# Performance work log

Hardware: AMD Instinct MI355X
Metric: run time of the kernel (lower is better)

## Reference

```python
import jax, jax.numpy as jnp
import numpy as np

N = 50000      # nodes per graph (= num hyperedges, forced by the stack ops)
E = 800000     # incidence pairs per graph
L = 16         # max nodes per hyperedge (padded with index 0)
F_IN = 128     # in_channels
D1 = 256       # dim_1
D2 = D1 // 4   # conv2 out dim = FusionAttention in_size
H_ATT = 128    # FusionAttention hidden_size
EPS = 1e-15


def setup_inputs() -> dict:
    key = jax.random.key(0)
    ks = jax.random.split(key, 32)
    inp = {}
    for i in range(4):
        inp[f"x{i}"] = jax.random.normal(ks[i], (N, F_IN), jnp.float32)
        nidx = jax.random.randint(ks[4 + i], (E,), 0, N, dtype=jnp.int32)
        eidx = jax.random.randint(ks[8 + i], (E,), 0, N, dtype=jnp.int32)
        inp[f"ei{i}"] = jnp.stack([nidx, eidx])  # [2, E]
        hn = jax.random.randint(ks[12 + i], (N, L), 0, N + 1, dtype=jnp.int32)
        inp[f"hnode{i}"] = hn
        # hye_len = number of real (non-padding) entries per hyperedge
        inp[f"hlen{i}"] = jnp.sum(hn > 0, axis=1, keepdims=True).astype(jnp.float32)
    # shared Hgnn params (PyG HypergraphConv: lin without bias + separate bias)
    inp["W1"] = jax.random.normal(ks[16], (F_IN, D1), jnp.float32) / np.sqrt(F_IN).astype(np.float32)
    inp["b1"] = jnp.zeros((D1,), jnp.float32)
    inp["W2"] = jax.random.normal(ks[17], (D1, D2), jnp.float32) / np.sqrt(D1).astype(np.float32)
    inp["b2"] = jnp.zeros((D2,), jnp.float32)
    # two FusionAttention heads: Linear(D2,H_ATT)+Tanh, Linear(H_ATT,1,bias=False)
    for name, a, b in [("ac", 18, 19), ("am", 20, 21)]:
        inp[f"{name}_W1"] = jax.random.normal(ks[a], (D2, H_ATT), jnp.float32) / np.sqrt(D2).astype(np.float32)
        inp[f"{name}_b1"] = jnp.zeros((H_ATT,), jnp.float32)
        inp[f"{name}_W2"] = jax.random.normal(ks[b], (H_ATT, 1), jnp.float32) / np.sqrt(H_ATT).astype(np.float32)
    return inp


def _hconv(x, node_idx, edge_idx, W, b):
    """PyG HypergraphConv (heads=1, unit hyperedge weights):
    X' = D^-1 H B^-1 H^T (X W) + b, via two segment-sum passes."""
    x = x @ W  # [N, out]
    ones = jnp.ones(node_idx.shape, x.dtype)
    deg_n = jax.ops.segment_sum(ones, node_idx, num_segments=N)
    d_inv = jnp.where(deg_n > 0, 1.0 / deg_n, 0.0)
    deg_e = jax.ops.segment_sum(ones, edge_idx, num_segments=N)
    b_inv = jnp.where(deg_e > 0, 1.0 / deg_e, 0.0)
    # node -> hyperedge: m_e = B^-1[e] * sum_{v in e} x[v]
    efeat = b_inv[:, None] * jax.ops.segment_sum(x[node_idx], edge_idx, num_segments=N)
    # hyperedge -> node: out_v = D^-1[v] * sum_{e : v in e} m_e
    out = d_inv[:, None] * jax.ops.segment_sum(efeat[edge_idx], node_idx, num_segments=N)
    return out + b


def _hgnn(x, ei, W1, b1, W2, b2):
    x = jax.nn.relu(_hconv(x, ei[0], ei[1], W1, b1))
    return jax.nn.relu(_hconv(x, ei[0], ei[1], W2, b2))


def _hye_emb(node_emb, hlen, hnode):
    # prepend zero row so padding index 0 gathers zeros
    padded = jnp.concatenate([jnp.zeros((1, node_emb.shape[1]), node_emb.dtype), node_emb], axis=0)
    seq = padded[hnode]                    # [M, L, F]
    return jnp.sum(seq, axis=1) / (hlen + EPS)


def _fusion_attn(z, W1, b1, W2):
    # z: [N, 4, d]
    w = (jnp.tanh(z @ W1 + b1) @ W2).mean(0)      # [4, 1]
    beta = jax.nn.softmax(w, axis=0)              # [4, 1]
    return jnp.sum(beta * z, axis=1)              # [N, d]


def reference(x0, x1, x2, x3, ei0, ei1, ei2, ei3,
              hlen0, hlen1, hlen2, hlen3, hnode0, hnode1, hnode2, hnode3,
              W1, b1, W2, b2, ac_W1, ac_b1, ac_W2, am_W1, am_b1, am_W2):
    x1_cm = _hgnn(x0, ei0, W1, b1, W2, b2)
    x1_mc = _hgnn(x1, ei1, W1, b1, W2, b2)
    x1_cc = _hgnn(x2, ei2, W1, b1, W2, b2)
    x1_mm = _hgnn(x3, ei3, W1, b1, W2, b2)
    x2_cm = _hye_emb(x1_cm, hlen0, hnode0)
    x2_mc = _hye_emb(x1_mc, hlen1, hnode1)
    x2_cc = _hye_emb(x1_cc, hlen2, hnode2)
    x2_mm = _hye_emb(x1_mm, hlen3, hnode3)
    x_c = jnp.stack((x1_mc, x2_cm, x1_cc, x2_cc), axis=1)  # [N, 4, D2]
    x_m = jnp.stack((x1_cm, x2_mc, x1_mm, x2_mm), axis=1)
    h_c = _fusion_attn(x_c, ac_W1, ac_b1, ac_W2)
    h_m = _fusion_attn(x_m, am_W1, am_b1, am_W2)
    return (h_c, h_m)
```

## Files before the change

### kernel.cpp

```cpp
#include <hip/hip_runtime.h>
#include <hip/hip_bf16.h>

#define NF   128
#define DD1  256
#define DD2  64
#define HATT 128

static inline int cdiv(int a, int b) { return (a + b - 1) / b; }

__global__ __launch_bounds__(256) void count_rank(const int* __restrict__ nidx,
                                                  const int* __restrict__ eidx,
                                                  int* __restrict__ deg,
                                                  int* __restrict__ rank,
                                                  int N, int E) {
    int e = blockIdx.x * 256 + threadIdx.x;
    if (e < E) {
        const int vn = nidx[e], ve = eidx[e];
        const int rn = atomicAdd(&deg[vn], 1);
        const int re = atomicAdd(&deg[N + ve], 1);
        rank[e] = rn | (re << 16);
    }
}

__global__ __launch_bounds__(256) void scan_blocks(const int* __restrict__ in,
                                                   int* __restrict__ out,
                                                   int* __restrict__ partials, int n) {
    __shared__ int s[256];
    const int base = blockIdx.x * 1024;
    const int t = threadIdx.x;
    int v[4], sum = 0;
#pragma unroll
    for (int i = 0; i < 4; i++) {
        const int idx = base + t * 4 + i;
        v[i] = (idx < n) ? in[idx] : 0;
        sum += v[i];
    }
    s[t] = sum;
    __syncthreads();
    for (int o = 1; o < 256; o <<= 1) {
        int x = 0;
        if (t >= o) x = s[t - o];
        __syncthreads();
        if (t >= o) s[t] += x;
        __syncthreads();
    }
    if (t == 255) partials[blockIdx.x] = s[255];
    int run = (t == 0) ? 0 : s[t - 1];
#pragma unroll
    for (int i = 0; i < 4; i++) {
        const int idx = base + t * 4 + i;
        if (idx < n) out[idx] = run;
        run += v[i];
    }
}

__global__ __launch_bounds__(256) void scan_partials(int* __restrict__ partials, int P) {
    __shared__ int s[256];
    const int t = threadIdx.x;
    s[t] = (t < P) ? partials[t] : 0;
    __syncthreads();
    for (int o = 1; o < 256; o <<= 1) {
        int x = 0;
        if (t >= o) x = s[t - o];
        __syncthreads();
        if (t >= o) s[t] += x;
        __syncthreads();
    }
    if (t < P) partials[t] = (t == 0) ? 0 : s[t - 1];
}

__global__ __launch_bounds__(256) void scan_add(int* __restrict__ off,
                                                const int* __restrict__ partials,
                                                int n, int total) {
    const int idx = blockIdx.x * 256 + threadIdx.x;
    if (idx < n) off[idx] += partials[idx >> 10];
    if (idx == 0) off[n] = total;
}

__global__ __launch_bounds__(256) void build_fill(const int* __restrict__ nidx,
                                                  const int* __restrict__ eidx,
                                                  const int* __restrict__ rank,
                                                  const int* __restrict__ off,
                                                  int* __restrict__ srcidx,
                                                  int N, int E, int shardSize) {
    const int shard = blockIdx.x & 7;
    const int chunk = blockIdx.x >> 3;
    const int lo = shard * shardSize;
    const int hi = lo + shardSize;
    const int base = chunk * 1024;
#pragma unroll
    for (int i = 0; i < 4; i++) {
        const int e = base + i * 256 + threadIdx.x;
        if (e < E) {
            const int vn = nidx[e], ve = eidx[e];
            const int rk = rank[e];
            if (vn >= lo && vn < hi)
                srcidx[off[vn] + (rk & 0xffff)] = ve;
            if (ve >= lo && ve < hi)
                srcidx[off[N + ve] + (rk >> 16)] = vn;
        }
    }
}

__global__ __launch_bounds__(256) void invert_deg_int(const int* __restrict__ deg,
                                                      float* __restrict__ inv, int n) {
    int t = blockIdx.x * 256 + threadIdx.x;
    if (t < n) {
        const int v = deg[t];
        inv[t] = (v > 0) ? 1.0f / (float)v : 0.f;
    }
}

__global__ __launch_bounds__(256) void gather_rows_128(const float* __restrict__ src,
                                                       const int* __restrict__ off,
                                                       const int* __restrict__ srcidx,
                                                       const float* __restrict__ scale,
                                                       float* __restrict__ dst, int Nn) {
    const int row = blockIdx.x * 16 + (threadIdx.x >> 4);
    if (row >= Nn) return;
    const int c = (threadIdx.x & 15) << 2;
    const int j0 = off[row], j1 = off[row + 1];
    float4 pa = make_float4(0.f, 0.f, 0.f, 0.f);
    float4 pb = make_float4(0.f, 0.f, 0.f, 0.f);
    float4 qa = make_float4(0.f, 0.f, 0.f, 0.f);
    float4 qb = make_float4(0.f, 0.f, 0.f, 0.f);
    int j = j0;
    for (; j + 3 < j1; j += 4) {
        const int s0 = srcidx[j + 0];
        const int s1 = srcidx[j + 1];
        const int s2 = srcidx[j + 2];
        const int s3 = srcidx[j + 3];
        const float4 v0a = *(const float4*)&src[(size_t)s0 * 128 + c];
        const float4 v0b = *(const float4*)&src[(size_t)s0 * 128 + c + 64];
        const float4 v1a = *(const float4*)&src[(size_t)s1 * 128 + c];
        const float4 v1b = *(const float4*)&src[(size_t)s1 * 128 + c + 64];
        const float4 v2a = *(const float4*)&src[(size_t)s2 * 128 + c];
        const float4 v2b = *(const float4*)&src[(size_t)s2 * 128 + c + 64];
        const float4 v3a = *(const float4*)&src[(size_t)s3 * 128 + c];
        const float4 v3b = *(const float4*)&src[(size_t)s3 * 128 + c + 64];
        pa.x += v0a.x + v1a.x; pa.y += v0a.y + v1a.y;
        pa.z += v0a.z + v1a.z; pa.w += v0a.w + v1a.w;
        qa.x += v2a.x + v3a.x; qa.y += v2a.y + v3a.y;
        qa.z += v2a.z + v3a.z; qa.w += v2a.w + v3a.w;
        pb.x += v0b.x + v1b.x; pb.y += v0b.y + v1b.y;
        pb.z += v0b.z + v1b.z; pb.w += v0b.w + v1b.w;
        qb.x += v2b.x + v3b.x; qb.y += v2b.y + v3b.y;
        qb.z += v2b.z + v3b.z; qb.w += v2b.w + v3b.w;
    }
    for (; j < j1; j++) {
        const int s0 = srcidx[j];
        const float4 va = *(const float4*)&src[(size_t)s0 * 128 + c];
        const float4 vb = *(const float4*)&src[(size_t)s0 * 128 + c + 64];
        pa.x += va.x; pa.y += va.y; pa.z += va.z; pa.w += va.w;
        pb.x += vb.x; pb.y += vb.y; pb.z += vb.z; pb.w += vb.w;
    }
    float4 aca = make_float4(pa.x + qa.x, pa.y + qa.y, pa.z + qa.z, pa.w + qa.w);
    float4 acb = make_float4(pb.x + qb.x, pb.y + qb.y, pb.z + qb.z, pb.w + qb.w);
    if (scale) {
        const float s = scale[row];
        aca.x *= s; aca.y *= s; aca.z *= s; aca.w *= s;
        acb.x *= s; acb.y *= s; acb.z *= s; acb.w *= s;
    }
    *(float4*)&dst[(size_t)row * 128 + c] = aca;
    *(float4*)&dst[(size_t)row * 128 + c + 64] = acb;
}

__global__ __launch_bounds__(256) void gather_rows_64(const float* __restrict__ src,
                                                      const int* __restrict__ off,
                                                      const int* __restrict__ srcidx,
                                                      const float* __restrict__ scale,
                                                      const float* __restrict__ post_bias,
                                                      float* __restrict__ dst, int Nn) {
    const int row = blockIdx.x * 32 + (threadIdx.x >> 3);
    if (row >= Nn) return;
    const int c = (threadIdx.x & 7) << 2;
    const int j0 = off[row], j1 = off[row + 1];
    float4 pa = make_float4(0.f, 0.f, 0.f, 0.f);
    float4 pb = make_float4(0.f, 0.f, 0.f, 0.f);
    float4 qa = make_float4(0.f, 0.f, 0.f, 0.f);
    float4 qb = make_float4(0.f, 0.f, 0.f, 0.f);
    int j = j0;
    for (; j + 3 < j1; j += 4) {
        const int s0 = srcidx[j + 0];
        const int s1 = srcidx[j + 1];
        const int s2 = srcidx[j + 2];
        const int s3 = srcidx[j + 3];
        const float4 v0a = *(const float4*)&src[(size_t)s0 * 64 + c];
        const float4 v0b = *(const float4*)&src[(size_t)s0 * 64 + c + 32];
        const float4 v1a = *(const float4*)&src[(size_t)s1 * 64 + c];
        const float4 v1b = *(const float4*)&src[(size_t)s1 * 64 + c + 32];
        const float4 v2a = *(const float4*)&src[(size_t)s2 * 64 + c];
        const float4 v2b = *(const float4*)&src[(size_t)s2 * 64 + c + 32];
        const float4 v3a = *(const float4*)&src[(size_t)s3 * 64 + c];
        const float4 v3b = *(const float4*)&src[(size_t)s3 * 64 + c + 32];
        pa.x += v0a.x + v1a.x; pa.y += v0a.y + v1a.y;
        pa.z += v0a.z + v1a.z; pa.w += v0a.w + v1a.w;
        qa.x += v2a.x + v3a.x; qa.y += v2a.y + v3a.y;
        qa.z += v2a.z + v3a.z; qa.w += v2a.w + v3a.w;
        pb.x += v0b.x + v1b.x; pb.y += v0b.y + v1b.y;
        pb.z += v0b.z + v1b.z; pb.w += v0b.w + v1b.w;
        qb.x += v2b.x + v3b.x; qb.y += v2b.y + v3b.y;
        qb.z += v2b.z + v3b.z; qb.w += v2b.w + v3b.w;
    }
    for (; j < j1; j++) {
        const int s0 = srcidx[j];
        const float4 va = *(const float4*)&src[(size_t)s0 * 64 + c];
        const float4 vb = *(const float4*)&src[(size_t)s0 * 64 + c + 32];
        pa.x += va.x; pa.y += va.y; pa.z += va.z; pa.w += va.w;
        pb.x += vb.x; pb.y += vb.y; pb.z += vb.z; pb.w += vb.w;
    }
    float4 aca = make_float4(pa.x + qa.x, pa.y + qa.y, pa.z + qa.z, pa.w + qa.w);
    float4 acb = make_float4(pb.x + qb.x, pb.y + qb.y, pb.z + qb.z, pb.w + qb.w);
    if (scale) {
        const float s = scale[row];
        aca.x *= s; aca.y *= s; aca.z *= s; aca.w *= s;
        acb.x *= s; acb.y *= s; acb.z *= s; acb.w *= s;
    }
    if (post_bias) {
        aca.x = fmaxf(aca.x + post_bias[c + 0], 0.f);
        aca.y = fmaxf(aca.y + post_bias[c + 1], 0.f);
        aca.z = fmaxf(aca.z + post_bias[c + 2], 0.f);
        aca.w = fmaxf(aca.w + post_bias[c + 3], 0.f);
        acb.x = fmaxf(acb.x + post_bias[c + 32], 0.f);
        acb.y = fmaxf(acb.y + post_bias[c + 33], 0.f);
        acb.z = fmaxf(acb.z + post_bias[c + 34], 0.f);
        acb.w = fmaxf(acb.w + post_bias[c + 35], 0.f);
    }
    *(float4*)&dst[(size_t)row * 64 + c] = aca;
    *(float4*)&dst[(size_t)row * 64 + c + 32] = acb;
}

__global__ __launch_bounds__(256) void gemm1_f32(const float* __restrict__ A,
                                                 const float* __restrict__ B,
                                                 float* __restrict__ C, int M,
                                                 const float* __restrict__ dinv,
                                                 const float* __restrict__ bias) {
    __shared__ float As[32][132];
    __shared__ float Bs[32][128];
    const int tid = threadIdx.x;
    const int m0 = blockIdx.y * 128;
    const int bn = blockIdx.x * 128;
    const int rq = (tid >> 4) << 2;
    const int cq = (tid & 15) << 2;

    float acc[8][8] = {{0.f}};

    for (int k0 = 0; k0 < 128; k0 += 32) {
#pragma unroll
        for (int i = 0; i < 4; i++) {
            const int f = tid + 256 * i;
            const int r = f >> 3;
            const int q = (f & 7) << 2;
            const int grow = m0 + r;
            float4 v = make_float4(0.f, 0.f, 0.f, 0.f);
            if (grow < M) v = *(const float4*)&A[(size_t)grow * 128 + k0 + q];
            As[q + 0][r] = v.x;
            As[q + 1][r] = v.y;
            As[q + 2][r] = v.z;
            As[q + 3][r] = v.w;
        }
#pragma unroll
        for (int i = 0; i < 4; i++) {
            const int f = tid + 256 * i;
            const int r = f >> 5;
            const int c4 = (f & 31) << 2;
            *(float4*)&Bs[r][c4] = *(const float4*)&B[(size_t)(k0 + r) * 256 + bn + c4];
        }
        __syncthreads();
#pragma unroll
        for (int k = 0; k < 32; k++) {
            float av[8], bv[8];
            *(float4*)&av[0] = *(const float4*)&As[k][rq];
            *(float4*)&av[4] = *(const float4*)&As[k][rq + 64];
            *(float4*)&bv[0] = *(const float4*)&Bs[k][cq];
            *(float4*)&bv[4] = *(const float4*)&Bs[k][cq + 64];
#pragma unroll
            for (int r = 0; r < 8; r++)
#pragma unroll
                for (int c = 0; c < 8; c++)
                    acc[r][c] = fmaf(av[r], bv[c], acc[r][c]);
        }
        __syncthreads();
    }
#pragma unroll
    for (int r = 0; r < 8; r++) {
        const int grow = m0 + rq + (r & 3) + ((r >> 2) << 6);
        if (grow < M) {
            const float s = dinv[grow];
            float o[8];
#pragma unroll
            for (int c = 0; c < 4; c++)
                o[c] = fmaxf(fmaf(acc[r][c], s, bias[bn + cq + c]), 0.f);
#pragma unroll
            for (int c = 4; c < 8; c++)
                o[c] = fmaxf(fmaf(acc[r][c], s, bias[bn + 64 + cq + (c - 4)]), 0.f);
            *(float4*)&C[(size_t)grow * 256 + bn + cq] = *(float4*)&o[0];
            *(float4*)&C[(size_t)grow * 256 + bn + 64 + cq] = *(float4*)&o[4];
        }
    }
}

__global__ __launch_bounds__(256) void gemm2_f32(const float* __restrict__ A,
                                                 const float* __restrict__ B,
                                                 float* __restrict__ C, int M) {
    __shared__ float As[32][132];
    __shared__ float Bs[32][64];
    const int tid = threadIdx.x;
    const int m0 = blockIdx.y * 128;
    const int tr = (tid >> 3) << 2;
    const int tc = (tid & 7) << 3;

    float acc[4][8] = {{0.f}};

    for (int k0 = 0; k0 < 256; k0 += 32) {
#pragma unroll
        for (int i = 0; i < 4; i++) {
            const int f = tid + 256 * i;
            const int r = f >> 3;
            const int q = (f & 7) << 2;
            const int grow = m0 + r;
            float4 v = make_float4(0.f, 0.f, 0.f, 0.f);
            if (grow < M) v = *(const float4*)&A[(size_t)grow * 256 + k0 + q];
            As[q + 0][r] = v.x;
            As[q + 1][r] = v.y;
            As[q + 2][r] = v.z;
            As[q + 3][r] = v.w;
        }
#pragma unroll
        for (int i = 0; i < 2; i++) {
            const int f = tid + 256 * i;
            const int r = f >> 4;
            const int c4 = (f & 15) << 2;
            *(float4*)&Bs[r][c4] = *(const float4*)&B[(size_t)(k0 + r) * 64 + c4];
        }
        __syncthreads();
#pragma unroll
        for (int k = 0; k < 32; k++) {
            float av[4], bv[8];
            *(float4*)&av[0] = *(const float4*)&As[k][tr];
            *(float4*)&bv[0] = *(const float4*)&Bs[k][tc];
            *(float4*)&bv[4] = *(const float4*)&Bs[k][tc + 4];
#pragma unroll
            for (int r = 0; r < 4; r++)
#pragma unroll
                for (int c = 0; c < 8; c++)
                    acc[r][c] = fmaf(av[r], bv[c], acc[r][c]);
        }
        __syncthreads();
    }
#pragma unroll
    for (int r = 0; r < 4; r++) {
        const int grow = m0 + tr + r;
        if (grow < M) {
            *(float4*)&C[(size_t)grow * 64 + tc] =
                make_float4(acc[r][0], acc[r][1], acc[r][2], acc[r][3]);
            *(float4*)&C[(size_t)grow * 64 + tc + 4] =
                make_float4(acc[r][4], acc[r][5], acc[r][6], acc[r][7]);
        }
    }
}

__global__ __launch_bounds__(256) void hye_emb_kernel(const float* __restrict__ emb,
                                                      const int* __restrict__ hnode,
                                                      const float* __restrict__ hlen,
                                                      float* __restrict__ out, int Nn) {
    const int r = blockIdx.x * 16 + (threadIdx.x >> 4);
    const int c = (threadIdx.x & 15) << 2;
    if (r >= Nn) return;
    const int4* hp4 = (const int4*)&hnode[(size_t)r * 16];
    const int4 w0 = hp4[0], w1 = hp4[1], w2 = hp4[2], w3 = hp4[3];
    int idx[16] = {w0.x, w0.y, w0.z, w0.w, w1.x, w1.y, w1.z, w1.w,
                   w2.x, w2.y, w2.z, w2.w, w3.x, w3.y, w3.z, w3.w};
    float4 a0 = make_float4(0.f, 0.f, 0.f, 0.f);
    float4 a1 = make_float4(0.f, 0.f, 0.f, 0.f);
    float4 a2 = make_float4(0.f, 0.f, 0.f, 0.f);
    float4 a3 = make_float4(0.f, 0.f, 0.f, 0.f);
#pragma unroll
    for (int l = 0; l < 16; l += 4) {
        if (idx[l + 0] > 0) {
            const float4 v = *(const float4*)&emb[(size_t)(idx[l + 0] - 1) * 64 + c];
            a0.x += v.x; a0.y += v.y; a0.z += v.z; a0.w += v.w;
        }
        if (idx[l + 1] > 0) {
            const float4 v = *(const float4*)&emb[(size_t)(idx[l + 1] - 1) * 64 + c];
            a1.x += v.x; a1.y += v.y; a1.z += v.z; a1.w += v.w;
        }
        if (idx[l + 2] > 0) {
            const float4 v = *(const float4*)&emb[(size_t)(idx[l + 2] - 1) * 64 + c];
            a2.x += v.x; a2.y += v.y; a2.z += v.z; a2.w += v.w;
        }
        if (idx[l + 3] > 0) {
            const float4 v = *(const float4*)&emb[(size_t)(idx[l + 3] - 1) * 64 + c];
            a3.x += v.x; a3.y += v.y; a3.z += v.z; a3.w += v.w;
        }
    }
    const float inv = 1.0f / (hlen[r] + 1e-15f);
    float4 acc;
    acc.x = (a0.x + a1.x + a2.x + a3.x) * inv;
    acc.y = (a0.y + a1.y + a2.y + a3.y) * inv;
    acc.z = (a0.z + a1.z + a2.z + a3.z) * inv;
    acc.w = (a0.w + a1.w + a2.w + a3.w) * inv;
    *(float4*)&out[(size_t)r * 64 + c] = acc;
}

struct AttnArgs {
    const float* z[8];
    const float* W1c; const float* b1c; const float* W2c;
    const float* W1m; const float* b1m; const float* W2m;
    float* accw;
    int Nn;
};

__global__ __launch_bounds__(256) void attn_gemm(AttnArgs a) {
    __shared__ float As[64][68];
    __shared__ float Bs[64][128];
    __shared__ float red[4];
    const int tid = threadIdx.x;
    const int gy = blockIdx.y;
    const int head = gy >> 2;
    const float* __restrict__ z  = a.z[gy];
    const float* __restrict__ W1 = head ? a.W1m : a.W1c;
    const float* __restrict__ b1 = head ? a.b1m : a.b1c;
    const float* __restrict__ W2 = head ? a.W2m : a.W2c;
    const int m0 = blockIdx.x * 64;

    {
        const int m = tid >> 2;
        const int qb = tid & 3;
        const int grow = m0 + m;
#pragma unroll
        for (int it = 0; it < 4; it++) {
            const int q = qb + 4 * it;
            float4 v = make_float4(0.f, 0.f, 0.f, 0.f);
            if (grow < a.Nn) v = *(const float4*)&z[(size_t)grow * 64 + q * 4];
            As[q * 4 + 0][m] = v.x;
            As[q * 4 + 1][m] = v.y;
            As[q * 4 + 2][m] = v.z;
            As[q * 4 + 3][m] = v.w;
        }
    }
    {
#pragma unroll
        for (int i = 0; i < 8; i++) {
            const int f = tid + 256 * i;
            const int r = f >> 5, cc = (f & 31) << 2;
            *(float4*)&Bs[r][cc] = *(const float4*)&W1[(size_t)r * 128 + cc];
        }
    }
    __syncthreads();

    const int mq = (tid & 15) << 2;
    const int cq = (tid >> 4) << 2;
    float acc[4][8] = {{0.f}};
    for (int k = 0; k < 64; k++) {
        float av[4], bv[8];
        *(float4*)&av[0] = *(const float4*)&As[k][mq];
        *(float4*)&bv[0] = *(const float4*)&Bs[k][cq];
        *(float4*)&bv[4] = *(const float4*)&Bs[k][cq + 64];
#pragma unroll
        for (int r = 0; r < 4; r++)
#pragma unroll
            for (int c = 0; c < 8; c++)
                acc[r][c] = fmaf(av[r], bv[c], acc[r][c]);
    }

    float w2v[8], b1v[8];
#pragma unroll
    for (int c = 0; c < 8; c++) {
        const int col = cq + (c & 3) + ((c >> 2) << 6);
        w2v[c] = W2[col];
        b1v[c] = b1[col];
    }
    float local = 0.f;
#pragma unroll
    for (int r = 0; r < 4; r++) {
        if (m0 + mq + r < a.Nn) {
#pragma unroll
            for (int c = 0; c < 8; c++) {
                float s = acc[r][c] + b1v[c];
                s = fminf(fmaxf(s, -15.f), 15.f);
                const float t = __expf(2.f * s);
                local += (1.f - 2.f / (t + 1.f)) * w2v[c];
            }
        }
    }
#pragma unroll
    for (int off = 32; off >= 1; off >>= 1) local += __shfl_down(local, off, 64);
    if ((tid & 63) == 0) red[tid >> 6] = local;
    __syncthreads();
    if (tid == 0) atomicAdd(&a.accw[gy], red[0] + red[1] + red[2] + red[3]);
}

__global__ void softmax_beta(const float* __restrict__ acc, float* __restrict__ beta,
                             float invN) {
    const int t = threadIdx.x;
    if (t < 2) {
        const float* a = acc + 4 * t;
        float* b = beta + 4 * t;
        float w[4], m = -1e30f;
#pragma unroll
        for (int i = 0; i < 4; i++) { w[i] = a[i] * invN; m = fmaxf(m, w[i]); }
        float s = 0.f;
#pragma unroll
        for (int i = 0; i < 4; i++) { w[i] = expf(w[i] - m); s += w[i]; }
#pragma unroll
        for (int i = 0; i < 4; i++) b[i] = w[i] / s;
    }
}

__global__ __launch_bounds__(256) void weighted_sum(const float* __restrict__ z0,
                                                    const float* __restrict__ z1,
                                                    const float* __restrict__ z2,
                                                    const float* __restrict__ z3,
                                                    const float* __restrict__ beta,
                                                    float* __restrict__ out, int Nn) {
    const int t = blockIdx.x * 256 + threadIdx.x;
    if (t >= Nn * 16) return;
    const float b0 = beta[0], b1 = beta[1], b2 = beta[2], b3 = beta[3];
    const float4 v0 = *(const float4*)&z0[(size_t)t * 4];
    const float4 v1 = *(const float4*)&z1[(size_t)t * 4];
    const float4 v2 = *(const float4*)&z2[(size_t)t * 4];
    const float4 v3 = *(const float4*)&z3[(size_t)t * 4];
    float4 o;
    o.x = b0 * v0.x + b1 * v1.x + b2 * v2.x + b3 * v3.x;
    o.y = b0 * v0.y + b1 * v1.y + b2 * v2.y + b3 * v3.y;
    o.z = b0 * v0.z + b1 * v1.z + b2 * v2.z + b3 * v3.z;
    o.w = b0 * v0.w + b1 * v1.w + b2 * v2.w + b3 * v3.w;
    *(float4*)&out[(size_t)t * 4] = o;
}

extern "C" void kernel_launch(void* const* d_in, const int* in_sizes, int n_in,
                              void* d_out, int out_size, void* d_ws, size_t ws_size,
                              hipStream_t stream) {
    const int Nn = in_sizes[0] / NF;
    const int E  = in_sizes[1] / 2;
    const int N2 = 2 * Nn;

    const float* x[4];
    const int*   ei[4];
    const int*   hnode[4];
    const float* hlen[4];
    for (int g = 0; g < 4; g++) {
        x[g]     = (const float*)d_in[4 * g + 0];
        ei[g]    = (const int*)d_in[4 * g + 1];
        hnode[g] = (const int*)d_in[4 * g + 2];
        hlen[g]  = (const float*)d_in[4 * g + 3];
    }
    const float* W1   = (const float*)d_in[16];
    const float* b1   = (const float*)d_in[17];
    const float* W2   = (const float*)d_in[18];
    const float* b2   = (const float*)d_in[19];
    const float* acW1 = (const float*)d_in[20];
    const float* acb1 = (const float*)d_in[21];
    const float* acW2 = (const float*)d_in[22];
    const float* amW1 = (const float*)d_in[23];
    const float* amb1 = (const float*)d_in[24];
    const float* amW2 = (const float*)d_in[25];

    float* ws = (float*)d_ws;
    size_t o = 0;
    float* bufA = ws + o; o += (size_t)Nn * DD1;
    float* bufB = ws + o; o += (size_t)Nn * DD1;
    float* dinv = ws + o; o += N2;
    float* h2[4];
    float* hemb[4];
    for (int g = 0; g < 4; g++) { h2[g]   = ws + o; o += (size_t)Nn * DD2; }
    for (int g = 0; g < 4; g++) { hemb[g] = ws + o; o += (size_t)Nn * DD2; }
    float* accw = ws + o; o += 8;
    float* beta = ws + o; o += 8;
    int* iws = (int*)(ws + o);
    size_t io = 0;
    int* deg_i    = iws + io; io += N2;
    int* off      = iws + io; io += N2 + 1;
    int* partials = iws + io; io += 256;
    int* rank     = iws + io; io += E;
    int* srcidx   = iws + io; io += (size_t)2 * E;

    const int nScanBlocks = cdiv(N2, 1024);
    const int shardSize = cdiv(Nn, 8);

    for (int g = 0; g < 4; g++) {
        const int* nidx = ei[g];
        const int* eidx = ei[g] + E;
        const int* off_n = off;
        const int* off_e = off + Nn;
        const float* d_inv = dinv;
        const float* b_inv = dinv + Nn;

        hipMemsetAsync(deg_i, 0, (size_t)N2 * sizeof(int), stream);
        count_rank<<<cdiv(E, 256), 256, 0, stream>>>(nidx, eidx, deg_i, rank, Nn, E);
        scan_blocks<<<nScanBlocks, 256, 0, stream>>>(deg_i, off, partials, N2);
        scan_partials<<<1, 256, 0, stream>>>(partials, nScanBlocks);
        scan_add<<<cdiv(N2, 256), 256, 0, stream>>>(off, partials, N2, 2 * E);
        build_fill<<<8 * cdiv(E, 1024), 256, 0, stream>>>(nidx, eidx, rank, off,
                                                          srcidx, Nn, E, shardSize);
        invert_deg_int<<<cdiv(N2, 256), 256, 0, stream>>>(deg_i, dinv, N2);

        gather_rows_128<<<cdiv(Nn, 16), 256, 0, stream>>>(x[g], off_e, srcidx, b_inv, bufB, Nn);
        gather_rows_128<<<cdiv(Nn, 16), 256, 0, stream>>>(bufB, off_n, srcidx, nullptr, bufA, Nn);
        gemm1_f32<<<dim3(2, cdiv(Nn, 128)), 256, 0, stream>>>(bufA, W1, bufB, Nn, d_inv, b1);

        gemm2_f32<<<dim3(1, cdiv(Nn, 128)), 256, 0, stream>>>(bufB, W2, bufA, Nn);
        gather_rows_64<<<cdiv(Nn, 32), 256, 0, stream>>>(bufA, off_e, srcidx, b_inv,
                                                         nullptr, bufB, Nn);
        gather_rows_64<<<cdiv(Nn, 32), 256, 0, stream>>>(bufB, off_n, srcidx, d_inv,
                                                         b2, h2[g], Nn);

        hye_emb_kernel<<<cdiv(Nn, 16), 256, 0, stream>>>(h2[g], hnode[g], hlen[g], hemb[g], Nn);
    }

    hipMemsetAsync(accw, 0, 8 * sizeof(float), stream);
    AttnArgs aa;
    aa.z[0] = h2[1]; aa.z[1] = hemb[0]; aa.z[2] = h2[2]; aa.z[3] = hemb[2];
    aa.z[4] = h2[0]; aa.z[5] = hemb[1]; aa.z[6] = h2[3]; aa.z[7] = hemb[3];
    aa.W1c = acW1; aa.b1c = acb1; aa.W2c = acW2;
    aa.W1m = amW1; aa.b1m = amb1; aa.W2m = amW2;
    aa.accw = accw; aa.Nn = Nn;
    attn_gemm<<<dim3(cdiv(Nn, 64), 8), 256, 0, stream>>>(aa);
    softmax_beta<<<1, 64, 0, stream>>>(accw, beta, 1.0f / (float)Nn);

    float* out = (float*)d_out;
    weighted_sum<<<cdiv(Nn * 16, 256), 256, 0, stream>>>(h2[1], hemb[0], h2[2], hemb[2],
                                                         beta + 0, out, Nn);
    weighted_sum<<<cdiv(Nn * 16, 256), 256, 0, stream>>>(h2[0], hemb[1], h2[3], hemb[3],
                                                         beta + 4, out + (size_t)Nn * DD2, Nn);
}
```

Baseline: 1.870 ms.

## Batch all four graphs into single kernel launches per stage

Adds batched versions of the CSR build, both gathers, both GEMMs and the hyperedge embedding, each using a graph index (grid y or row/Nn) so that one launch covers all four graphs instead of looping per graph. This removes roughly forty launches and fills the GPU better for small stages such as the scans and GEMM tails. The batched path is taken only when the workspace is large enough, since it needs about four times the intermediate buffers; otherwise the old per-graph loop still runs. The prefix scan now spans 4*2N entries, so scan_partials grows to 512 threads.

```diff
diff --git a/kernel.cpp b/kernel.cpp
--- a/kernel.cpp
+++ b/kernel.cpp
@@ -54,12 +54,12 @@
     }
 }
 
-__global__ __launch_bounds__(256) void scan_partials(int* __restrict__ partials, int P) {
-    __shared__ int s[256];
+__global__ __launch_bounds__(512) void scan_partials(int* __restrict__ partials, int P) {
+    __shared__ int s[512];
     const int t = threadIdx.x;
     s[t] = (t < P) ? partials[t] : 0;
     __syncthreads();
-    for (int o = 1; o < 256; o <<= 1) {
+    for (int o = 1; o < 512; o <<= 1) {
         int x = 0;
         if (t >= o) x = s[t - o];
         __syncthreads();
@@ -108,6 +108,53 @@
     if (t < n) {
         const int v = deg[t];
         inv[t] = (v > 0) ? 1.0f / (float)v : 0.f;
+    }
+}
+
+struct BuildB {
+    const int* nidx[4];
+    const int* eidx[4];
+    int* deg;
+    int* rank;
+    const int* off;
+    int* srcidx;
+    int Nn, E, shardSize;
+};
+
+__global__ __launch_bounds__(256) void count_rank_b(BuildB a) {
+    const int g = blockIdx.y;
+    const int e = blockIdx.x * 256 + threadIdx.x;
+    if (e < a.E) {
+        const int vn = a.nidx[g][e], ve = a.eidx[g][e];
+        int* dg = a.deg + (size_t)g * 2 * a.Nn;
+        const int rn = atomicAdd(&dg[vn], 1);
+        const int re = atomicAdd(&dg[a.Nn + ve], 1);
+        a.rank[(size_t)g * a.E + e] = rn | (re << 16);
+    }
+}
+
+__global__ __launch_bounds__(256) void build_fill_b(BuildB a) {
+    const int g = blockIdx.y;
+    const int shard = blockIdx.x & 7;
+    const int chunk = blockIdx.x >> 3;
+    const int lo = shard * a.shardSize;
+    const int hi = lo + a.shardSize;
+    const int base = chunk * 1024;
+    const int* __restrict__ nidx = a.nidx[g];
+    const int* __restrict__ eidx = a.eidx[g];
+    const int* __restrict__ rank = a.rank + (size_t)g * a.E;
+    const int* __restrict__ off  = a.off + (size_t)g * 2 * a.Nn;
+#pragma unroll
+    for (int i = 0; i < 4; i++) {
+        const int e = base + i * 256 + threadIdx.x;
+        if (e < a.E) {
+            const int vn = nidx[e], ve = eidx[e];
+            const int rk = rank[e];
+            if (vn >= lo && vn < hi)
+                a.srcidx[off[vn] + (rk & 0xffff)] = ve;
+            if (ve >= lo && ve < hi)
+                a.srcidx[off[a.Nn + ve] + (rk >> 16)] = vn;
+        }
     }
 }
 
@@ -163,6 +210,70 @@
     }
     *(float4*)&dst[(size_t)row * 128 + c] = aca;
     *(float4*)&dst[(size_t)row * 128 + c + 64] = acb;
+}
+
+struct Gather128B {
+    const float* src[4];
+    float* dst;
+    const int* off;
+    const int* srcidx;
+    const float* dinv;
+    int passBase;
+    int Nn;
+};
+
+__global__ __launch_bounds__(256) void gather128_b(Gather128B a) {
+    const int gr = blockIdx.x * 16 + (threadIdx.x >> 4);
+    if (gr >= 4 * a.Nn) return;
+    const int g = gr / a.Nn;
+    const int row = gr - g * a.Nn;
+    const float* __restrict__ src = a.src[g];
+    const int ob = g * 2 * a.Nn + a.passBase + row;
+    const int c = (threadIdx.x & 15) << 2;
+    const int j0 = a.off[ob], j1 = a.off[ob + 1];
+    float4 pa = make_float4(0.f, 0.f, 0.f, 0.f);
+    float4 pb = make_float4(0.f, 0.f, 0.f, 0.f);
+    float4 qa = make_float4(0.f, 0.f, 0.f, 0.f);
+    float4 qb = make_float4(0.f, 0.f, 0.f, 0.f);
+    int j = j0;
+    for (; j + 3 < j1; j += 4) {
+        const int s0 = a.srcidx[j + 0];
+        const int s1 = a.srcidx[j + 1];
+        const int s2 = a.srcidx[j + 2];
+        const int s3 = a.srcidx[j + 3];
+        const float4 v0a = *(const float4*)&src[(size_t)s0 * 128 + c];
+        const float4 v0b = *(const float4*)&src[(size_t)s0 * 128 + c + 64];
+        const float4 v1a = *(const float4*)&src[(size_t)s1 * 128 + c];
+        const float4 v1b = *(const float4*)&src[(size_t)s1 * 128 + c + 64];
+        const float4 v2a = *(const float4*)&src[(size_t)s2 * 128 + c];
+        const float4 v2b = *(const float4*)&src[(size_t)s2 * 128 + c + 64];
+        const float4 v3a = *(const float4*)&src[(size_t)s3 * 128 + c];
+        const float4 v3b = *(const float4*)&src[(size_t)s3 * 128 + c + 64];
+        pa.x += v0a.x + v1a.x; pa.y += v0a.y + v1a.y;
+        pa.z += v0a.z + v1a.z; pa.w += v0a.w + v1a.w;
+        qa.x += v2a.x + v3a.x; qa.y += v2a.y + v3a.y;
+        qa.z += v2a.z + v3a.z; qa.w += v2a.w + v3a.w;
+        pb.x += v0b.x + v1b.x; pb.y += v0b.y + v1b.y;
+        pb.z += v0b.z + v1b.z; pb.w += v0b.w + v1b.w;
+        qb.x += v2b.x + v3b.x; qb.y += v2b.y + v3b.y;
+        qb.z += v2b.z + v3b.z; qb.w += v2b.w + v3b.w;
+    }
+    for (; j < j1; j++) {
+        const int s0 = a.srcidx[j];
+        const float4 va = *(const float4*)&src[(size_t)s0 * 128 + c];
+        const float4 vb = *(const float4*)&src[(size_t)s0 * 128 + c + 64];
+        pa.x += va.x; pa.y += va.y; pa.z += va.z; pa.w += va.w;
+        pb.x += vb.x; pb.y += vb.y; pb.z += vb.z; pb.w += vb.w;
+    }
+    float4 aca = make_float4(pa.x + qa.x, pa.y + qa.y, pa.z + qa.z, pa.w + qa.w);
+    float4 acb = make_float4(pb.x + qb.x, pb.y + qb.y, pb.z + qb.z, pb.w + qb.w);
+    if (a.dinv) {
+        const float s = a.dinv[ob];
+        aca.x *= s; aca.y *= s; aca.z *= s; aca.w *= s;
+        acb.x *= s; acb.y *= s; acb.z *= s; acb.w *= s;
+    }
+    *(float4*)&a.dst[(size_t)gr * 128 + c] = aca;
+    *(float4*)&a.dst[(size_t)gr * 128 + c + 64] = acb;
 }
 
 __global__ __launch_bounds__(256) void gather_rows_64(const float* __restrict__ src,
@@ -230,6 +341,81 @@
     *(float4*)&dst[(size_t)row * 64 + c + 32] = acb;
 }
 
+struct Gather64B {
+    const float* src[4];
+    float* dst;
+    const int* off;
+    const int* srcidx;
+    const float* dinv;
+    const float* post_bias;
+    int passBase;
+    int Nn;
+};
+
+__global__ __launch_bounds__(256) void gather64_b(Gather64B a) {
+    const int gr = blockIdx.x * 32 + (threadIdx.x >> 3);
+    if (gr >= 4 * a.Nn) return;
+    const int g = gr / a.Nn;
+    const int row = gr - g * a.Nn;
+    const float* __restrict__ src = a.src[g];
+    const int ob = g * 2 * a.Nn + a.passBase + row;
+    const int c = (threadIdx.x & 7) << 2;
+    const int j0 = a.off[ob], j1 = a.off[ob + 1];
+    float4 pa = make_float4(0.f, 0.f, 0.f, 0.f);
+    float4 pb = make_float4(0.f, 0.f, 0.f, 0.f);
+    float4 qa = make_float4(0.f, 0.f, 0.f, 0.f);
+    float4 qb = make_float4(0.f, 0.f, 0.f, 0.f);
+    int j = j0;
+    for (; j + 3 < j1; j += 4) {
+        const int s0 = a.srcidx[j + 0];
+        const int s1 = a.srcidx[j + 1];
+        const int s2 = a.srcidx[j + 2];
+        const int s3 = a.srcidx[j + 3];
+        const float4 v0a = *(const float4*)&src[(size_t)s0 * 64 + c];
+        const float4 v0b = *(const float4*)&src[(size_t)s0 * 64 + c + 32];
+        const float4 v1a = *(const float4*)&src[(size_t)s1 * 64 + c];
+        const float4 v1b = *(const float4*)&src[(size_t)s1 * 64 + c + 32];
+        const float4 v2a = *(const float4*)&src[(size_t)s2 * 64 + c];
+        const float4 v2b = *(const float4*)&src[(size_t)s2 * 64 + c + 32];
+        const float4 v3a = *(const float4*)&src[(size_t)s3 * 64 + c];
+        const float4 v3b = *(const float4*)&src[(size_t)s3 * 64 + c + 32];
+        pa.x += v0a.x + v1a.x; pa.y += v0a.y + v1a.y;
+        pa.z += v0a.z + v1a.z; pa.w += v0a.w + v1a.w;
+        qa.x += v2a.x + v3a.x; qa.y += v2a.y + v3a.y;
+        qa.z += v2a.z + v3a.z; qa.w += v2a.w + v3a.w;
+        pb.x += v0b.x + v1b.x; pb.y += v0b.y + v1b.y;
+        pb.z += v0b.z + v1b.z; pb.w += v0b.w + v1b.w;
+        qb.x += v2b.x + v3b.x; qb.y += v2b.y + v3b.y;
+        qb.z += v2b.z + v3b.z; qb.w += v2b.w + v3b.w;
+    }
+    for (; j < j1; j++) {
+        const int s0 = a.srcidx[j];
+        const float4 va = *(const float4*)&src[(size_t)s0 * 64 + c];
+        const float4 vb = *(const float4*)&src[(size_t)s0 * 64 + c + 32];
+        pa.x += va.x; pa.y += va.y; pa.z += va.z; pa.w += va.w;
+        pb.x += vb.x; pb.y += vb.y; pb.z += vb.z; pb.w += vb.w;
+    }
+    float4 aca = make_float4(pa.x + qa.x, pa.y + qa.y, pa.z + qa.z, pa.w + qa.w);
+    float4 acb = make_float4(pb.x + qb.x, pb.y + qb.y, pb.z + qb.z, pb.w + qb.w);
+    if (a.dinv) {
+        const float s = a.dinv[ob];
+        aca.x *= s; aca.y *= s; aca.z *= s; aca.w *= s;
+        acb.x *= s; acb.y *= s; acb.z *= s; acb.w *= s;
+    }
+    if (a.post_bias) {
+        aca.x = fmaxf(aca.x + a.post_bias[c + 0], 0.f);
+        aca.y = fmaxf(aca.y + a.post_bias[c + 1], 0.f);
+        aca.z = fmaxf(aca.z + a.post_bias[c + 2], 0.f);
+        aca.w = fmaxf(aca.w + a.post_bias[c + 3], 0.f);
+        acb.x = fmaxf(acb.x + a.post_bias[c + 32], 0.f);
+        acb.y = fmaxf(acb.y + a.post_bias[c + 33], 0.f);
+        acb.z = fmaxf(acb.z + a.post_bias[c + 34], 0.f);
+        acb.w = fmaxf(acb.w + a.post_bias[c + 35], 0.f);
+    }
+    *(float4*)&a.dst[(size_t)gr * 64 + c] = aca;
+    *(float4*)&a.dst[(size_t)gr * 64 + c + 32] = acb;
+}
+
 __global__ __launch_bounds__(256) void gemm1_f32(const float* __restrict__ A,
                                                  const float* __restrict__ B,
                                                  float* __restrict__ C, int M,
@@ -300,6 +486,85 @@
     }
 }
 
+struct Gemm1B {
+    const float* A;
+    const float* B;
+    float* C[4];
+    const float* dinv;
+    const float* bias;
+    int Nn;
+};
+
+__global__ __launch_bounds__(256) void gemm1_b(Gemm1B a) {
+    __shared__ float As[32][132];
+    __shared__ float Bs[32][128];
+    const int M = 4 * a.Nn;
+    const int tid = threadIdx.x;
+    const int m0 = blockIdx.y * 128;
+    const int bn = blockIdx.x * 128;
+    const int rq = (tid >> 4) << 2;
+    const int cq = (tid & 15) << 2;
+
+    float acc[8][8] = {{0.f}};
+
+    for (int k0 = 0; k0 < 128; k0 += 32) {
+#pragma unroll
+        for (int i = 0; i < 4; i++) {
+            const int f = tid + 256 * i;
+            const int r = f >> 3;
+            const int q = (f & 7) << 2;
+            const int grow = m0 + r;
+            float4 v = make_float4(0.f, 0.f, 0.f, 0.f);
+            if (grow < M) v = *(const float4*)&a.A[(size_t)grow * 128 + k0 + q];
+            As[q + 0][r] = v.x;
+            As[q + 1][r] = v.y;
+            As[q + 2][r] = v.z;
+            As[q + 3][r] = v.w;
+        }
+#pragma unroll
+        for (int i = 0; i < 4; i++) {
+            const int f = tid + 256 * i;
+            const int r = f >> 5;
+            const int c4 = (f & 31) << 2;
+            *(float4*)&Bs[r][c4] = *(const float4*)&a.B[(size_t)(k0 + r) * 256 + bn + c4];
+        }
+        __syncthreads();
+#pragma unroll
+        for (int k = 0; k < 32; k++) {
+            float av[8], bv[8];
+            *(float4*)&av[0] = *(const float4*)&As[k][rq];
+            *(float4*)&av[4] = *(const float4*)&As[k][rq + 64];
+            *(float4*)&bv[0] = *(const float4*)&Bs[k][cq];
+            *(float4*)&bv[4] = *(const float4*)&Bs[k][cq + 64];
+#pragma unroll
+            for (int r = 0; r < 8; r++)
+#pragma unroll
+                for (int c = 0; c < 8; c++)
+                    acc[r][c] = fmaf(av[r], bv[c], acc[r][c]);
+        }
+        __syncthreads();
+    }
+#pragma unroll
+    for (int r = 0; r < 8; r++) {
+        const int grow = m0 + rq + (r & 3) + ((r >> 2) << 6);
+        if (grow < M) {
+            const int g = grow / a.Nn;
+            const int lr = grow - g * a.Nn;
+            const float s = a.dinv[(size_t)g * 2 * a.Nn + lr];
+            float* Cg = a.C[g] + (size_t)lr * 256;
+            float o[8];
+#pragma unroll
+            for (int c = 0; c < 4; c++)
+                o[c] = fmaxf(fmaf(acc[r][c], s, a.bias[bn + cq + c]), 0.f);
+#pragma unroll
+            for (int c = 4; c < 8; c++)
+                o[c] = fmaxf(fmaf(acc[r][c], s, a.bias[bn + 64 + cq + (c - 4)]), 0.f);
+            *(float4*)&Cg[bn + cq] = *(float4*)&o[0];
+            *(float4*)&Cg[bn + 64 + cq] = *(float4*)&o[4];
+        }
+    }
+}
+
 __global__ __launch_bounds__(256) void gemm2_f32(const float* __restrict__ A,
                                                  const float* __restrict__ B,
                                                  float* __restrict__ C, int M) {
@@ -355,6 +620,76 @@
             *(float4*)&C[(size_t)grow * 64 + tc] =
                 make_float4(acc[r][0], acc[r][1], acc[r][2], acc[r][3]);
             *(float4*)&C[(size_t)grow * 64 + tc + 4] =
+                make_float4(acc[r][4], acc[r][5], acc[r][6], acc[r][7]);
+        }
+    }
+}
+
+struct Gemm2B {
+    const float* A[4];
+    const float* B;
+    float* C;
+    int Nn;
+};
+
+__global__ __launch_bounds__(256) void gemm2_b(Gemm2B a) {
+    __shared__ float As[32][132];
+    __shared__ float Bs[32][64];
+    const int M = 4 * a.Nn;
+    const int tid = threadIdx.x;
+    const int m0 = blockIdx.y * 128;
+    const int tr = (tid >> 3) << 2;
+    const int tc = (tid & 7) << 3;
+
+    float acc[4][8] = {{0.f}};
+
+    for (int k0 = 0; k0 < 256; k0 += 32) {
+#pragma unroll
+        for (int i = 0; i < 4; i++) {
+            const int f = tid + 256 * i;
+            const int r = f >> 3;
+            const int q = (f & 7) << 2;
+            const int grow = m0 + r;
+            float4 v = make_float4(0.f, 0.f, 0.f, 0.f);
+            if (grow < M) {
+                const int g = grow / a.Nn;
+                const int lr = grow - g * a.Nn;
+                v = *(const float4*)&a.A[g][(size_t)lr * 256 + k0 + q];
+            }
+            As[q + 0][r] = v.x;
+            As[q + 1][r] = v.y;
+            As[q + 2][r] = v.z;
+            As[q + 3][r] = v.w;
+        }
+#pragma unroll
+        for (int i = 0; i < 2; i++) {
+            const int f = tid + 256 * i;
+            const int r = f >> 4;
+            const int c4 = (f & 15) << 2;
+            *(float4*)&Bs[r][c4] = *(const float4*)&a.B[(size_t)(k0 + r) * 64 + c4];
+        }
+        __syncthreads();
+#pragma unroll
+        for (int k = 0; k < 32; k++) {
+            float av[4], bv[8];
+            *(float4*)&av[0] = *(const float4*)&As[k][tr];
+            *(float4*)&bv[0] = *(const float4*)&Bs[k][tc];
+            *(float4*)&bv[4] = *(const float4*)&Bs[k][tc + 4];
+#pragma unroll
+            for (int r = 0; r < 4; r++)
+#pragma unroll
+                for (int c = 0; c < 8; c++)
+                    acc[r][c] = fmaf(av[r], bv[c], acc[r][c]);
+        }
+        __syncthreads();
+    }
+#pragma unroll
+    for (int r = 0; r < 4; r++) {
+        const int grow = m0 + tr + r;
+        if (grow < M) {
+            *(float4*)&a.C[(size_t)grow * 64 + tc] =
+                make_float4(acc[r][0], acc[r][1], acc[r][2], acc[r][3]);
+            *(float4*)&a.C[(size_t)grow * 64 + tc + 4] =
                 make_float4(acc[r][4], acc[r][5], acc[r][6], acc[r][7]);
         }
     }
@@ -401,6 +736,57 @@
     acc.z = (a0.z + a1.z + a2.z + a3.z) * inv;
     acc.w = (a0.w + a1.w + a2.w + a3.w) * inv;
     *(float4*)&out[(size_t)r * 64 + c] = acc;
+}
+
+struct HyeB {
+    const float* emb;
+    const int* hnode[4];
+    const float* hlen[4];
+    float* out;
+    int Nn;
+};
+
+__global__ __launch_bounds__(256) void hye_b(HyeB a) {
+    const int gr = blockIdx.x * 16 + (threadIdx.x >> 4);
+    const int c = (threadIdx.x & 15) << 2;
+    if (gr >= 4 * a.Nn) return;
+    const int g = gr / a.Nn;
+    const int lr = gr - g * a.Nn;
+    const float* __restrict__ emb = a.emb + (size_t)g * a.Nn * 64;
+    const int4* hp4 = (const int4*)&a.hnode[g][(size_t)lr * 16];
+    const int4 w0 = hp4[0], w1 = hp4[1], w2 = hp4[2], w3 = hp4[3];
+    int idx[16] = {w0.x, w0.y, w0.z, w0.w, w1.x, w1.y, w1.z, w1.w,
+                   w2.x, w2.y, w2.z, w2.w, w3.x, w3.y, w3.z, w3.w};
+    float4 a0 = make_float4(0.f, 0.f, 0.f, 0.f);
+    float4 a1 = make_float4(0.f, 0.f, 0.f, 0.f);
+    float4 a2 = make_float4(0.f, 0.f, 0.f, 0.f);
+    float4 a3 = make_float4(0.f, 0.f, 0.f, 0.f);
+#pragma unroll
+    for (int l = 0; l < 16; l += 4) {
+        if (idx[l + 0] > 0) {
+            const float4 v = *(const float4*)&emb[(size_t)(idx[l + 0] - 1) * 64 + c];
+            a0.x += v.x; a0.y += v.y; a0.z += v.z; a0.w += v.w;
+        }
+        if (idx[l + 1] > 0) {
+            const float4 v = *(const float4*)&emb[(size_t)(idx[l + 1] - 1) * 64 + c];
+            a1.x += v.x; a1.y += v.y; a1.z += v.z; a1.w += v.w;
+        }
+        if (idx[l + 2] > 0) {
+            const float4 v = *(const float4*)&emb[(size_t)(idx[l + 2] - 1) * 64 + c];
+            a2.x += v.x; a2.y += v.y; a2.z += v.z; a2.w += v.w;
+        }
+        if (idx[l + 3] > 0) {
+            const float4 v = *(const float4*)&emb[(size_t)(idx[l + 3] - 1) * 64 + c];
+            a3.x += v.x; a3.y += v.y; a3.z += v.z; a3.w += v.w;
+        }
+    }
+    const float inv = 1.0f / (a.hlen[g][lr] + 1e-15f);
+    float4 acc;
+    acc.x = (a0.x + a1.x + a2.x + a3.x) * inv;
+    acc.y = (a0.y + a1.y + a2.y + a3.y) * inv;
+    acc.z = (a0.z + a1.z + a2.z + a3.z) * inv;
+    acc.w = (a0.w + a1.w + a2.w + a3.w) * inv;
+    *(float4*)&a.out[(size_t)gr * 64 + c] = acc;
 }
 
 struct AttnArgs {
@@ -557,6 +943,116 @@
     const float* amb1 = (const float*)d_in[24];
     const float* amW2 = (const float*)d_in[25];
 
+    const size_t fB1   = (size_t)4 * Nn * 128;
+    const size_t fB2   = (size_t)4 * Nn * 128;
+    const size_t fH2   = (size_t)4 * Nn * 64;
+    const size_t fHE   = (size_t)4 * Nn * 64;
+    const size_t fDinv = (size_t)4 * N2;
+    const size_t fcnt  = fB1 + fB2 + fH2 + fHE + fDinv + 16;
+    const size_t icnt  = (size_t)4 * N2 + ((size_t)4 * N2 + 4) + 512 +
+                         (size_t)4 * E + (size_t)8 * E;
+    const size_t need  = (fcnt + icnt) * sizeof(float) + 1024;
+
+    if (need <= ws_size) {
+        float* ws = (float*)d_ws;
+        size_t o = 0;
+        float* B1    = ws + o; o += fB1;
+        float* B2    = ws + o; o += fB2;
+        float* h2b   = ws + o; o += fH2;
+        float* hembb = ws + o; o += fHE;
+        float* dinv  = ws + o; o += fDinv;
+        float* accw  = ws + o; o += 8;
+        float* beta  = ws + o; o += 8;
+        int* iws = (int*)(ws + o);
+        size_t io = 0;
+        int* deg      = iws + io; io += (size_t)4 * N2;
+        int* off      = iws + io; io += (size_t)4 * N2 + 4;
+        int* partials = iws + io; io += 512;
+        int* rank     = iws + io; io += (size_t)4 * E;
+        int* srcidx   = iws + io; io += (size_t)8 * E;
+
+        float* C1p[4] = { B1, B1 + (size_t)Nn * 256, h2b, hembb };
+        float* Dbuf = B2;
+        float* E1   = B2 + (size_t)Nn * 256;
+
+        const int n8  = 4 * N2;
+        const int nScanBlocks = cdiv(n8, 1024);
+
+        BuildB bb;
+        for (int g = 0; g < 4; g++) { bb.nidx[g] = ei[g]; bb.eidx[g] = ei[g] + E; }
+        bb.deg = deg; bb.rank = rank; bb.off = off; bb.srcidx = srcidx;
+        bb.Nn = Nn; bb.E = E; bb.shardSize = cdiv(Nn, 8);
+
+        hipMemsetAsync(deg, 0, (size_t)n8 * sizeof(int), stream);
+        count_rank_b<<<dim3(cdiv(E, 256), 4), 256, 0, stream>>>(bb);
+        scan_blocks<<<nScanBlocks, 256, 0, stream>>>(deg, off, partials, n8);
+        scan_partials<<<1, 512, 0, stream>>>(partials, nScanBlocks);
+        scan_add<<<cdiv(n8, 256), 256, 0, stream>>>(off, partials, n8, 2 * 4 * E);
+        build_fill_b<<<dim3(8 * cdiv(E, 1024), 4), 256, 0, stream>>>(bb);
+        invert_deg_int<<<cdiv(n8, 256), 256, 0, stream>>>(deg, dinv, n8);
+
+        Gather128B g1;
+        for (int g = 0; g < 4; g++) g1.src[g] = x[g];
+        g1.dst = B1; g1.off = off; g1.srcidx = srcidx;
+        g1.dinv = dinv; g1.passBase = Nn; g1.Nn = Nn;
+        gather128_b<<<cdiv(4 * Nn, 16), 256, 0, stream>>>(g1);
+
+        Gather128B g2;
+        for (int g = 0; g < 4; g++) g2.src[g] = B1 + (size_t)g * Nn * 128;
+        g2.dst = B2; g2.off = off; g2.srcidx = srcidx;
+        g2.dinv = nullptr; g2.passBase = 0; g2.Nn = Nn;
+        gather128_b<<<cdiv(4 * Nn, 16), 256, 0, stream>>>(g2);
+
+        Gemm1B gm1;
+        gm1.A = B2; gm1.B = W1;
+        for (int g = 0; g < 4; g++) gm1.C[g] = C1p[g];
+        gm1.dinv = dinv; gm1.bias = b1; gm1.Nn = Nn;
+        gemm1_b<<<dim3(2, cdiv(4 * Nn, 128)), 256, 0, stream>>>(gm1);
+
+        Gemm2B gm2;
+        for (int g = 0; g < 4; g++) gm2.A[g] = C1p[g];
+        gm2.B = W2; gm2.C = Dbuf; gm2.Nn = Nn;
+        gemm2_b<<<dim3(1, cdiv(4 * Nn, 128)), 256, 0, stream>>>(gm2);
+
+        Gather64B g3;
+        for (int g = 0; g < 4; g++) g3.src[g] = Dbuf + (size_t)g * Nn * 64;
+        g3.dst = E1; g3.off = off; g3.srcidx = srcidx;
+        g3.dinv = dinv; g3.post_bias = nullptr; g3.passBase = Nn; g3.Nn = Nn;
+        gather64_b<<<cdiv(4 * Nn, 32), 256, 0, stream>>>(g3);
+
+        Gather64B g4;
+        for (int g = 0; g < 4; g++) g4.src[g] = E1 + (size_t)g * Nn * 64;
+        g4.dst = h2b; g4.off = off; g4.srcidx = srcidx;
+        g4.dinv = dinv; g4.post_bias = b2; g4.passBase = 0; g4.Nn = Nn;
+        gather64_b<<<cdiv(4 * Nn, 32), 256, 0, stream>>>(g4);
+
+        HyeB hb;
+        hb.emb = h2b;
+        for (int g = 0; g < 4; g++) { hb.hnode[g] = hnode[g]; hb.hlen[g] = hlen[g]; }
+        hb.out = hembb; hb.Nn = Nn;
+        hye_b<<<cdiv(4 * Nn, 16), 256, 0, stream>>>(hb);
+
+        const size_t st = (size_t)Nn * 64;
+        hipMemsetAsync(accw, 0, 8 * sizeof(float), stream);
+        AttnArgs aa;
+        aa.z[0] = h2b + 1 * st; aa.z[1] = hembb + 0 * st;
+        aa.z[2] = h2b + 2 * st; aa.z[3] = hembb + 2 * st;
+        aa.z[4] = h2b + 0 * st; aa.z[5] = hembb + 1 * st;
+        aa.z[6] = h2b + 3 * st; aa.z[7] = hembb + 3 * st;
+        aa.W1c = acW1; aa.b1c = acb1; aa.W2c = acW2;
+        aa.W1m = amW1; aa.b1m = amb1; aa.W2m = amW2;
+        aa.accw = accw; aa.Nn = Nn;
+        attn_gemm<<<dim3(cdiv(Nn, 64), 8), 256, 0, stream>>>(aa);
+        softmax_beta<<<1, 64, 0, stream>>>(accw, beta, 1.0f / (float)Nn);
+
+        float* out = (float*)d_out;
+        weighted_sum<<<cdiv(Nn * 16, 256), 256, 0, stream>>>(
+            aa.z[0], aa.z[1], aa.z[2], aa.z[3], beta + 0, out, Nn);
+        weighted_sum<<<cdiv(Nn * 16, 256), 256, 0, stream>>>(
+            aa.z[4], aa.z[5], aa.z[6], aa.z[7], beta + 4, out + (size_t)Nn * DD2, Nn);
+        return;
+    }
+
     float* ws = (float*)d_ws;
     size_t o = 0;
     float* bufA = ws + o; o += (size_t)Nn * DD1;
@@ -572,7 +1068,7 @@
     size_t io = 0;
     int* deg_i    = iws + io; io += N2;
     int* off      = iws + io; io += N2 + 1;
-    int* partials = iws + io; io += 256;
+    int* partials = iws + io; io += 512;
     int* rank     = iws + io; io += E;
     int* srcidx   = iws + io; io += (size_t)2 * E;
 
@@ -590,7 +1086,7 @@
         hipMemsetAsync(deg_i, 0, (size_t)N2 * sizeof(int), stream);
         count_rank<<<cdiv(E, 256), 256, 0, stream>>>(nidx, eidx, deg_i, rank, Nn, E);
         scan_blocks<<<nScanBlocks, 256, 0, stream>>>(deg_i, off, partials, N2);
-        scan_partials<<<1, 256, 0, stream>>>(partials, nScanBlocks);
+        scan_partials<<<1, 512, 0, stream>>>(partials, nScanBlocks);
         scan_add<<<cdiv(N2, 256), 256, 0, stream>>>(off, partials, N2, 2 * E);
         build_fill<<<8 * cdiv(E, 1024), 256, 0, stream>>>(nidx, eidx, rank, off,
                                                           srcidx, Nn, E, shardSize);
```

Measured after the change: 1.875 ms. No clear change (+0.2%).
